# Kernel optimization log

Hardware: AMD Instinct MI355X
Metric: run time of the kernel (lower is better)

## Reference

```python
import jax, jax.numpy as jnp
import numpy as np

B, D_IN, E, H, V = 4096, 4096, 2048, 2048, 32000


def setup_inputs() -> dict:
    key = jax.random.key(0)
    ks = jax.random.split(key, 24)
    s = 0.02
    p = lambda k, shape: (jax.random.normal(k, shape, dtype=jnp.float32) * s)
    return {
        "input": jax.random.normal(ks[0], (B, D_IN), dtype=jnp.float32),
        "hidden": jnp.zeros((B, H), dtype=jnp.float32),
        "cell": jnp.zeros((B, H), dtype=jnp.float32),
        # embedding linear (input_size -> emb_size), stored as [in, out]
        "We": p(ks[1], (D_IN, E)), "be": p(ks[2], (E,)),
        # x-to-gate linears (emb -> hidden)
        "Wf": p(ks[3], (E, H)), "bf": p(ks[4], (H,)),
        "Wi": p(ks[5], (E, H)), "bi": p(ks[6], (H,)),
        "Wc": p(ks[7], (E, H)), "bc": p(ks[8], (H,)),
        "Wo": p(ks[9], (E, H)), "bo": p(ks[10], (H,)),
        # hidden-to-gate linears (hidden -> hidden)
        "Uf": p(ks[11], (H, H)), "bhf": p(ks[12], (H,)),
        "Ui": p(ks[13], (H, H)), "bhi": p(ks[14], (H,)),
        "Uc": p(ks[15], (H, H)), "bhc": p(ks[16], (H,)),
        "Uo": p(ks[17], (H, H)), "bho": p(ks[18], (H,)),
        # output head (hidden -> output_size)
        "Wend": p(ks[19], (H, V)), "bend": p(ks[20], (V,)),
    }


def reference(input, hidden, cell,
              We, be, Wf, bf, Wi, bi, Wc, bc, Wo, bo,
              Uf, bhf, Ui, bhi, Uc, bhc, Uo, bho, Wend, bend):
    # embedded = Linear(input)
    emb = input @ We + be                                  # [B, E]
    f = jax.nn.sigmoid(emb @ Wf + bf + hidden @ Uf + bhf)  # forget gate [B, H]
    i = jax.nn.sigmoid(emb @ Wi + bi + hidden @ Ui + bhi)  # input gate
    g = jnp.tanh(emb @ Wc + bc + hidden @ Uc + bhc)        # candidate cell
    new_cell = f * cell + i * g
    o = jax.nn.sigmoid(emb @ Wo + bo + hidden @ Uo + bho)  # output gate
    new_hidden = o * jnp.tanh(new_cell)
    out = jax.nn.log_softmax(new_hidden @ Wend + bend, axis=1)  # [B, V]
    return (out, new_hidden, new_cell)
```

## Files before the change

### kernel.cpp

```cpp
#include <hip/hip_runtime.h>
#include <stdint.h>

#define B_DIM 4096
#define DIN   4096
#define E_DIM 2048
#define H_DIM 2048
#define V_DIM 32000

typedef __attribute__((ext_vector_type(8))) short s8v;
typedef __attribute__((ext_vector_type(4))) float f4v;
typedef __attribute__((ext_vector_type(4))) int   i4v;
typedef __attribute__((ext_vector_type(8))) int   i8v;
typedef __attribute__((ext_vector_type(4))) uint  u4v;
typedef __attribute__((ext_vector_type(4))) float f4n;

__device__ __forceinline__ ushort f2bf(float f) {
    union { float f; uint32_t u; } v; v.f = f;
    uint32_t u = v.u;
    return (ushort)((u + 0x7FFFu + ((u >> 16) & 1u)) >> 16);
}
__device__ __forceinline__ float bf2f(ushort h) {
    union { uint32_t u; float f; } v; v.u = ((uint32_t)h) << 16;
    return v.f;
}

__device__ __forceinline__ uint8_t f2fp8(float x) {
    union { float f; uint32_t u; } v; v.f = x;
    uint8_t sign = (uint8_t)((v.u >> 24) & 0x80u);
    uint32_t a = v.u & 0x7FFFFFFFu;
    if (a >= 0x43E00000u) return sign | 0x7E;
    uint32_t r = a + 0x0007FFFFu + ((a >> 20) & 1u);
    int e = (int)(r >> 23) - 127 + 7;
    if (e <= 0) {
        float s = fabsf(x);
        int q = (int)(s * 512.0f + 0.5f);
        if (q > 7) q = 7;
        return sign | (uint8_t)q;
    }
    uint32_t m = (r >> 20) & 7u;
    uint8_t b = (uint8_t)((e << 3) | m);
    if (b == 0x7F) b = 0x7E;
    return sign | b;
}

__global__ void k_cvt(const float* __restrict__ src, ushort* __restrict__ dst, int n4) {
    int i = blockIdx.x * blockDim.x + threadIdx.x;
    if (i >= n4) return;
    float4 v = *(const float4*)(src + (size_t)i * 4);
    ushort4 o;
    o.x = f2bf(v.x); o.y = f2bf(v.y); o.z = f2bf(v.z); o.w = f2bf(v.w);
    *(ushort4*)(dst + (size_t)i * 4) = o;
}

__global__ void k_cvt_hidden(const float* __restrict__ src, ushort* __restrict__ dst) {
    int i = blockIdx.x * blockDim.x + threadIdx.x;
    int b = i >> 9;
    int c = (i & 511) << 2;
    float4 v = *(const float4*)(src + (size_t)b * H_DIM + c);
    ushort4 o;
    o.x = f2bf(v.x); o.y = f2bf(v.y); o.z = f2bf(v.z); o.w = f2bf(v.w);
    *(ushort4*)(dst + (size_t)b * 4096 + 2048 + c) = o;
}

__global__ void k_transpose_bf16(const float* __restrict__ src, ushort* __restrict__ dst,
                                 int srcCols, int dstStride, int dstRowOff, int dstColOff) {
    __shared__ float tile[32][33];
    int tx = threadIdx.x, ty = threadIdx.y;
    int n0 = blockIdx.x * 32, k0 = blockIdx.y * 32;
#pragma unroll
    for (int i = 0; i < 4; i++)
        tile[ty + 8 * i][tx] = src[(size_t)(k0 + ty + 8 * i) * srcCols + n0 + tx];
    __syncthreads();
#pragma unroll
    for (int i = 0; i < 4; i++) {
        int n = ty + 8 * i;
        dst[(size_t)(dstRowOff + n0 + n) * dstStride + dstColOff + k0 + tx] = f2bf(tile[tx][n]);
    }
}

__global__ void k_transpose_fp8(const float* __restrict__ src, uint8_t* __restrict__ dst,
                                int srcCols, int dstStride) {
    __shared__ float tile[32][33];
    int tx = threadIdx.x, ty = threadIdx.y;
    int n0 = blockIdx.x * 32, k0 = blockIdx.y * 32;
#pragma unroll
    for (int i = 0; i < 4; i++)
        tile[ty + 8 * i][tx] = src[(size_t)(k0 + ty + 8 * i) * srcCols + n0 + tx];
    __syncthreads();
#pragma unroll
    for (int i = 0; i < 4; i++) {
        int n = ty + 8 * i;
        dst[(size_t)(n0 + n) * dstStride + k0 + tx] = f2fp8(tile[tx][n] * 32.0f);
    }
}

__global__ void k_transpose_gate8(const float* __restrict__ W0, const float* __restrict__ W1,
                                  const float* __restrict__ W2, const float* __restrict__ W3,
                                  const float* __restrict__ U0, const float* __restrict__ U1,
                                  const float* __restrict__ U2, const float* __restrict__ U3,
                                  ushort* __restrict__ dst) {
    const float* srcs[8] = {W0, W1, W2, W3, U0, U1, U2, U3};
    int z = blockIdx.z;
    const float* src = srcs[z];
    int g = z & 3;
    int dstColOff = (z >> 2) << 11;
    __shared__ float tile[32][33];
    int tx = threadIdx.x, ty = threadIdx.y;
    int n0 = blockIdx.x * 32, k0 = blockIdx.y * 32;
#pragma unroll
    for (int i = 0; i < 4; i++)
        tile[ty + 8 * i][tx] = src[(size_t)(k0 + ty + 8 * i) * H_DIM + n0 + tx];
    __syncthreads();
#pragma unroll
    for (int i = 0; i < 4; i++) {
        int h = n0 + ty + 8 * i;
        int drow = ((h >> 6) << 8) + ((g >> 1) << 7) + (((h >> 4) & 3) << 5) + ((g & 1) << 4) + (h & 15);
        dst[(size_t)drow * 4096 + dstColOff + k0 + tx] = f2bf(tile[tx][ty + 8 * i]);
    }
}

__global__ void k_biaspack(const float* __restrict__ b0, const float* __restrict__ bh0,
                           const float* __restrict__ b1, const float* __restrict__ bh1,
                           const float* __restrict__ b2, const float* __restrict__ bh2,
                           const float* __restrict__ b3, const float* __restrict__ bh3,
                           float* __restrict__ out) {
    int h = blockIdx.x * blockDim.x + threadIdx.x;
    if (h >= H_DIM) return;
    int base = ((h >> 6) << 8) + (((h >> 4) & 3) << 5) + (h & 15);
    out[base]             = b0[h] + bh0[h];
    out[base + 16]        = b1[h] + bh1[h];
    out[base + 128]       = b2[h] + bh2[h];
    out[base + 128 + 16]  = b3[h] + bh3[h];
}

template<int OUT_BF16>
__global__ __launch_bounds__(256, 2)
void k_gemm_bt(const ushort* __restrict__ A, const ushort* __restrict__ Bt,
               void* __restrict__ Cv, const float* __restrict__ bias,
               int M, int N, int K, int lda, int ldb, int ldc) {
    __shared__ __align__(16) ushort ldsA[128 * 64];
    __shared__ __align__(16) ushort ldsB[128 * 64];
    const int t = threadIdx.x;
    const int wid = t >> 6, lane = t & 63;

    int nwg = gridDim.x;
    int bid = blockIdx.x;
    int wg  = (bid & 7) * (nwg >> 3) + (bid >> 3);
    int NT  = N >> 7;
    int mt  = wg / NT, nt = wg - mt * NT;
    int m0  = mt << 7, n0 = nt << 7;

    f4v acc[4][4];
#pragma unroll
    for (int i = 0; i < 4; i++)
#pragma unroll
        for (int j = 0; j < 4; j++) acc[i][j] = (f4v){0.f, 0.f, 0.f, 0.f};

    const int wr = wid >> 1, wc = wid & 1;

    const int kTiles = K >> 6;
    for (int kt = 0; kt < kTiles; ++kt) {
#pragma unroll
        for (int c = 0; c < 4; ++c) {
            int idx = c * 256 + wid * 64 + lane;
            int row = idx >> 3;
            int kb  = (idx & 7) << 4;
            const ushort* gA = A  + (size_t)(m0 + row) * lda + (kt << 6) + (kb >> 1);
            const ushort* gB = Bt + (size_t)(n0 + row) * ldb + (kt << 6) + (kb >> 1);
            char* lA = (char*)ldsA + (size_t)(c * 256 + wid * 64) * 16;
            char* lB = (char*)ldsB + (size_t)(c * 256 + wid * 64) * 16;
            __builtin_amdgcn_global_load_lds((const __attribute__((address_space(1))) void*)gA,
                                             (__attribute__((address_space(3))) void*)lA, 16, 0, 0);
            __builtin_amdgcn_global_load_lds((const __attribute__((address_space(1))) void*)gB,
                                             (__attribute__((address_space(3))) void*)lB, 16, 0, 0);
        }
        __syncthreads();

#pragma unroll
        for (int ks = 0; ks < 2; ++ks) {
            s8v af[4], bfr[4];
#pragma unroll
            for (int m = 0; m < 4; ++m) {
                int r = wr * 64 + m * 16 + (lane & 15);
                int kb = ks * 64 + ((lane >> 4) << 4);
                af[m] = *(const s8v*)((const char*)ldsA + r * 128 + kb);
            }
#pragma unroll
            for (int n = 0; n < 4; ++n) {
                int r = wc * 64 + n * 16 + (lane & 15);
                int kb = ks * 64 + ((lane >> 4) << 4);
                bfr[n] = *(const s8v*)((const char*)ldsB + r * 128 + kb);
            }
#pragma unroll
            for (int m = 0; m < 4; ++m)
#pragma unroll
                for (int n = 0; n < 4; ++n)
                    acc[m][n] = __builtin_amdgcn_mfma_f32_16x16x32_bf16(af[m], bfr[n], acc[m][n], 0, 0, 0);
        }
        __syncthreads();
    }

#pragma unroll
    for (int n = 0; n < 4; ++n) {
        int cg = n0 + wc * 64 + n * 16 + (lane & 15);
        float bv = bias[cg];
#pragma unroll
        for (int m = 0; m < 4; ++m) {
            int rbase = m0 + wr * 64 + m * 16 + ((lane >> 4) << 2);
#pragma unroll
            for (int r = 0; r < 4; ++r) {
                float v = acc[m][n][r] + bv;
                if (OUT_BF16)
                    ((ushort*)Cv)[(size_t)(rbase + r) * ldc + cg] = f2bf(v);
                else
                    ((float*)Cv)[(size_t)(rbase + r) * ldc + cg] = v;
            }
        }
    }
}

template<int EPI>
__global__ __launch_bounds__(512, 2)
void k_gemm256(const ushort* __restrict__ A, const ushort* __restrict__ Bt,
               void* __restrict__ Cv, const float* __restrict__ bias,
               int N, int K, int lda, int ldb, int ldc,
               const float* __restrict__ cell, float* __restrict__ outH,
               float* __restrict__ outC, uint8_t* __restrict__ hidF8,
               float2* __restrict__ partials, int ncb) {
    __shared__ __align__(16) ushort ldsA[2][256 * 64];
    __shared__ __align__(16) ushort ldsB[2][256 * 64];
    const int t = threadIdx.x;
    const int wid = t >> 6, lane = t & 63;
    const int wr = wid >> 2, wc = wid & 3;

    int nwg = gridDim.x, bid = blockIdx.x;
    int wg = (bid & 7) * (nwg >> 3) + (bid >> 3);
    int NT = N >> 8;
    int mt = wg / NT, nt = wg - mt * NT;
    int m0 = mt << 8, n0 = nt << 8;

    int offA[4], offB[4];
#pragma unroll
    for (int cc = 0; cc < 4; ++cc) {
        int idx = cc * 512 + t;
        int row = idx >> 3;
        int col = ((idx & 7) ^ (row & 7)) << 3;
        offA[cc] = (m0 + row) * lda + col;
        offB[cc] = (n0 + row) * ldb + col;
    }

#define GLOAD(GP, LP) __builtin_amdgcn_global_load_lds(                                   \
        (const __attribute__((address_space(1))) void*)(GP),                              \
        (__attribute__((address_space(3))) void*)(LP), 16, 0, 0)
#define STAGE_HA(BUF, KT, H) do {                                                         \
    GLOAD(A + offA[(H)*2]     + ((KT) << 6), &ldsA[BUF][(((H)*2)*512 + (wid<<6)) * 8]);   \
    GLOAD(A + offA[(H)*2 + 1] + ((KT) << 6), &ldsA[BUF][(((H)*2+1)*512 + (wid<<6)) * 8]); \
} while (0)
#define STAGE_HB(BUF, KT, H) do {                                                         \
    GLOAD(Bt + offB[(H)*2]     + ((KT) << 6), &ldsB[BUF][(((H)*2)*512 + (wid<<6)) * 8]);  \
    GLOAD(Bt + offB[(H)*2 + 1] + ((KT) << 6), &ldsB[BUF][(((H)*2+1)*512 + (wid<<6)) * 8]);\
} while (0)

    f4v acc[8][4];
#pragma unroll
    for (int i = 0; i < 8; i++)
#pragma unroll
        for (int j = 0; j < 4; j++) acc[i][j] = (f4v){0.f, 0.f, 0.f, 0.f};

    s8v af[4][2], bfA[2][2], bfB[2][2];
    const int swz = (lane & 7) << 4;
    const int kcol = (lane >> 4) << 4;

#define READ_A(BUF, MH) do {                                                              \
    _Pragma("unroll")                                                                     \
    for (int m_ = 0; m_ < 4; ++m_) {                                                      \
        int row = (MH)*128 + wr*64 + m_*16 + (lane & 15);                                 \
        _Pragma("unroll")                                                                 \
        for (int ks_ = 0; ks_ < 2; ++ks_)                                                 \
            af[m_][ks_] = *(const s8v*)((const char*)&ldsA[BUF][0] + row * 128 +          \
                                        ((ks_*64 + kcol) ^ swz));                         \
    } } while (0)
#define READ_B(BUF, NH, DST) do {                                                         \
    _Pragma("unroll")                                                                     \
    for (int n_ = 0; n_ < 2; ++n_) {                                                      \
        int row = (NH)*128 + wc*32 + n_*16 + (lane & 15);                                 \
        _Pragma("unroll")                                                                 \
        for (int ks_ = 0; ks_ < 2; ++ks_)                                                 \
            DST[n_][ks_] = *(const s8v*)((const char*)&ldsB[BUF][0] + row * 128 +         \
                                         ((ks_*64 + kcol) ^ swz));                        \
    } } while (0)
#define MFMA_Q(MH, NH, BF) do {                                                           \
    __builtin_amdgcn_s_setprio(1);                                                        \
    _Pragma("unroll")                                                                     \
    for (int m_ = 0; m_ < 4; ++m_)                                                        \
    _Pragma("unroll")                                                                     \
    for (int n_ = 0; n_ < 2; ++n_)                                                        \
    _Pragma("unroll")                                                                     \
    for (int ks_ = 0; ks_ < 2; ++ks_)                                                     \
        acc[(MH)*4 + m_][(NH)*2 + n_] = __builtin_amdgcn_mfma_f32_16x16x32_bf16(          \
            af[m_][ks_], BF[n_][ks_], acc[(MH)*4 + m_][(NH)*2 + n_], 0, 0, 0);            \
    __builtin_amdgcn_s_setprio(0);                                                        \
} while (0)
#define MEMBAR asm volatile("" ::: "memory")
#define BAR() do { MEMBAR; __builtin_amdgcn_s_barrier(); MEMBAR; } while (0)
#define WAITLGKM0() do { asm volatile("s_waitcnt lgkmcnt(0)" ::: "memory");               \
                         __builtin_amdgcn_sched_barrier(0); } while (0)

    const int kTiles = K >> 6;
    STAGE_HA(0, 0, 0); STAGE_HB(0, 0, 0); STAGE_HB(0, 0, 1); STAGE_HA(0, 0, 1);
    STAGE_HA(1, 1, 0); STAGE_HB(1, 1, 0); STAGE_HB(1, 1, 1); STAGE_HA(1, 1, 1);
    asm volatile("s_waitcnt vmcnt(6)" ::: "memory");
    BAR();

    for (int kt = 0; kt < kTiles; ++kt) {
        const int buf = kt & 1;
        const bool pf = (kt + 2 < kTiles);
        READ_A(buf, 0); READ_B(buf, 0, bfA);
        asm volatile("s_waitcnt lgkmcnt(8)" ::: "memory");
        BAR(); WAITLGKM0();
        MFMA_Q(0, 0, bfA);
        BAR();
        READ_B(buf, 1, bfB);
        if (pf) STAGE_HA(buf, kt + 2, 0);
        BAR(); WAITLGKM0();
        MFMA_Q(0, 1, bfB);
        BAR();
        READ_A(buf, 1);
        if (pf) STAGE_HB(buf, kt + 2, 0);
        BAR(); WAITLGKM0();
        MFMA_Q(1, 1, bfB);
        BAR();
        if (pf) { STAGE_HB(buf, kt + 2, 1); STAGE_HA(buf, kt + 2, 1); }
        MFMA_Q(1, 0, bfA);
        if (pf) asm volatile("s_waitcnt vmcnt(8)" ::: "memory");
        else    asm volatile("s_waitcnt vmcnt(0)" ::: "memory");
        BAR();
    }

    if (EPI == 0) {
    } else {
        int h = (n0 >> 2) + wc * 16 + (lane & 15);
        float bv[4];
#pragma unroll
        for (int j = 0; j < 4; ++j)
            bv[j] = bias[n0 + (j >> 1) * 128 + wc * 32 + (j & 1) * 16 + (lane & 15)];
#pragma unroll
        for (int mh = 0; mh < 2; ++mh)
#pragma unroll
        for (int m = 0; m < 4; ++m) {
            int rb = m0 + mh * 128 + wr * 64 + m * 16 + ((lane >> 4) << 2);
#pragma unroll
            for (int r = 0; r < 4; ++r) {
                int b = rb + r;
                float pf_ = acc[mh * 4 + m][0][r] + bv[0];
                float pi_ = acc[mh * 4 + m][1][r] + bv[1];
                float pc_ = acc[mh * 4 + m][2][r] + bv[2];
                float po_ = acc[mh * 4 + m][3][r] + bv[3];
                float fg = 1.f / (1.f + __expf(-pf_));
                float ig = 1.f / (1.f + __expf(-pi_));
                float gg = tanhf(pc_);
                float og = 1.f / (1.f + __expf(-po_));
                size_t off = (size_t)b * H_DIM + h;
                float nc = fg * cell[off] + ig * gg;
                float nh = og * tanhf(nc);
                outC[off] = nc;
                outH[off] = nh;
                hidF8[off] = f2fp8(nh * 8.0f);
            }
        }
    }
#undef GLOAD
#undef STAGE_HA
#undef STAGE_HB
#undef READ_A
#undef READ_B
#undef MFMA_Q
#undef MEMBAR
#undef BAR
#undef WAITLGKM0
}

__global__ __launch_bounds__(256, 3)
void k_gemm_mx(const uint8_t* __restrict__ A, const uint8_t* __restrict__ Bt,
               ushort* __restrict__ Lbf, const float* __restrict__ bias,
               float2* __restrict__ partials, int N, int K, int ldc, int ncb) {
    __shared__ __align__(16) uint8_t ldsA[128 * 128];
    __shared__ __align__(16) uint8_t ldsB[128 * 128];
    const int t = threadIdx.x;
    const int wid = t >> 6, lane = t & 63;
    const int wrr = wid >> 1, wcc = wid & 1;

    int bid = blockIdx.x;
    int mt  = ((bid & 7) << 2) | ((bid >> 3) & 3);
    int nt  = bid >> 5;
    int m0  = mt << 7, n0 = nt << 7;

    int offA[4], offB[4];
#pragma unroll
    for (int c = 0; c < 4; ++c) {
        int idx = c * 256 + t;
        int row = idx >> 3;
        int cb  = ((idx & 7) ^ (row & 7)) << 4;
        offA[c] = (m0 + row) * K + cb;
        offB[c] = (n0 + row) * K + cb;
    }

    f4v acc[4][4];
#pragma unroll
    for (int i = 0; i < 4; ++i)
#pragma unroll
        for (int j = 0; j < 4; ++j) acc[i][j] = (f4v){0.f, 0.f, 0.f, 0.f};

    const int l15 = lane & 15;
    const int sw  = (lane & 7) << 4;
    const int o0  = ((lane >> 4) << 5) ^ sw;
    const int o1  = o0 ^ 16;

    const int kTiles = K >> 7;
    for (int kt = 0; kt < kTiles; ++kt) {
#pragma unroll
        for (int c = 0; c < 4; ++c) {
            __builtin_amdgcn_global_load_lds(
                (const __attribute__((address_space(1))) void*)(A + offA[c] + (kt << 7)),
                (__attribute__((address_space(3))) void*)&ldsA[(c * 256 + wid * 64) * 16], 16, 0, 0);
            __builtin_amdgcn_global_load_lds(
                (const __attribute__((address_space(1))) void*)(Bt + offB[c] + (kt << 7)),
                (__attribute__((address_space(3))) void*)&ldsB[(c * 256 + wid * 64) * 16], 16, 0, 0);
        }
        __syncthreads();

        i8v af[4], bf[4];
#pragma unroll
        for (int m = 0; m < 4; ++m) {
            int row = wrr * 64 + m * 16 + l15;
            i4v lo = *(const i4v*)&ldsA[row * 128 + o0];
            i4v hi = *(const i4v*)&ldsA[row * 128 + o1];
            af[m] = __builtin_shufflevector(lo, hi, 0, 1, 2, 3, 4, 5, 6, 7);
        }
#pragma unroll
        for (int n = 0; n < 4; ++n) {
            int row = wcc * 64 + n * 16 + l15;
            i4v lo = *(const i4v*)&ldsB[row * 128 + o0];
            i4v hi = *(const i4v*)&ldsB[row * 128 + o1];
            bf[n] = __builtin_shufflevector(lo, hi, 0, 1, 2, 3, 4, 5, 6, 7);
        }
#pragma unroll
        for (int m = 0; m < 4; ++m)
#pragma unroll
            for (int n = 0; n < 4; ++n)
                acc[m][n] = __builtin_amdgcn_mfma_scale_f32_16x16x128_f8f6f4(
                    af[m], bf[n], acc[m][n], 0, 0, 0, 124, 0, 122);
        __syncthreads();
    }

    float bv[4];
#pragma unroll
    for (int n = 0; n < 4; ++n) bv[n] = bias[n0 + wcc * 64 + n * 16 + l15];
    float2* sm = (float2*)ldsA;
#pragma unroll
    for (int m = 0; m < 4; ++m) {
#pragma unroll
        for (int r = 0; r < 4; ++r) {
            int rl = wrr * 64 + m * 16 + ((lane >> 4) << 2) + r;
            float v[4];
#pragma unroll
            for (int n = 0; n < 4; ++n) v[n] = acc[m][n][r] + bv[n];
            size_t cr = (size_t)(m0 + rl) * ldc + n0 + wcc * 64 + l15;
            __builtin_nontemporal_store(f2bf(v[0]), &Lbf[cr]);
            __builtin_nontemporal_store(f2bf(v[1]), &Lbf[cr + 16]);
            __builtin_nontemporal_store(f2bf(v[2]), &Lbf[cr + 32]);
            __builtin_nontemporal_store(f2bf(v[3]), &Lbf[cr + 48]);
            float mx = fmaxf(fmaxf(v[0], v[1]), fmaxf(v[2], v[3]));
            float ss = __expf(v[0] - mx) + __expf(v[1] - mx) +
                       __expf(v[2] - mx) + __expf(v[3] - mx);
#pragma unroll
            for (int off = 1; off < 16; off <<= 1) {
                float mo = __shfl_xor(mx, off);
                float so = __shfl_xor(ss, off);
                float nm = fmaxf(mx, mo);
                ss = ss * __expf(mx - nm) + so * __expf(mo - nm);
                mx = nm;
            }
            if (l15 == 0) sm[wcc * 128 + rl] = make_float2(mx, ss);
        }
    }
    __syncthreads();
    if (t < 128) {
        float2 a = sm[t], b = sm[128 + t];
        float M = fmaxf(a.x, b.x);
        float S = a.y * __expf(a.x - M) + b.y * __expf(b.x - M);
        partials[(size_t)(m0 + t) * ncb + nt] = make_float2(M, S);
    }
}

__global__ void k_lsefin(const float2* __restrict__ part, float* __restrict__ lse, int ncb) {
    int row = blockIdx.x;
    int l = threadIdx.x;
    float M = -1e30f, S = 0.f;
    for (int i = l; i < ncb; i += 64) {
        float2 p = part[(size_t)row * ncb + i];
        float nm = fmaxf(M, p.x);
        S = S * __expf(M - nm) + p.y * __expf(p.x - nm);
        M = nm;
    }
#pragma unroll
    for (int off = 1; off < 64; off <<= 1) {
        float Mo = __shfl_xor(M, off);
        float So = __shfl_xor(S, off);
        float nm = fmaxf(M, Mo);
        S = S * __expf(M - nm) + So * __expf(Mo - nm);
        M = nm;
    }
    if (l == 0) lse[row] = M + logf(S);
}

__global__ void k_norm(const ushort* __restrict__ Lbf, const float* __restrict__ lse,
                       float* __restrict__ out) {
    int b = blockIdx.y;
    int c8 = blockIdx.x * blockDim.x + threadIdx.x;
    if (c8 >= V_DIM / 8) return;
    float l = lse[b];
    const u4v* src = (const u4v*)(Lbf + (size_t)b * V_DIM + (size_t)c8 * 8);
    u4v pv = __builtin_nontemporal_load(src);
    f4n q0, q1;
    q0.x = bf2f((ushort)(pv.x & 0xFFFF)) - l;
    q0.y = bf2f((ushort)(pv.x >> 16)) - l;
    q0.z = bf2f((ushort)(pv.y & 0xFFFF)) - l;
    q0.w = bf2f((ushort)(pv.y >> 16)) - l;
    q1.x = bf2f((ushort)(pv.z & 0xFFFF)) - l;
    q1.y = bf2f((ushort)(pv.z >> 16)) - l;
    q1.z = bf2f((ushort)(pv.w & 0xFFFF)) - l;
    q1.w = bf2f((ushort)(pv.w >> 16)) - l;
    float* dst = out + (size_t)b * V_DIM + (size_t)c8 * 8;
    __builtin_nontemporal_store(q0, (f4n*)dst);
    __builtin_nontemporal_store(q1, (f4n*)(dst + 4));
}

extern "C" void kernel_launch(void* const* d_in, const int* in_sizes, int n_in,
                              void* d_out, int out_size, void* d_ws, size_t ws_size,
                              hipStream_t stream) {
    const float* in_input  = (const float*)d_in[0];
    const float* in_hidden = (const float*)d_in[1];
    const float* in_cell   = (const float*)d_in[2];
    const float* We   = (const float*)d_in[3];
    const float* be   = (const float*)d_in[4];
    const float* Wf   = (const float*)d_in[5];
    const float* bfv  = (const float*)d_in[6];
    const float* Wi   = (const float*)d_in[7];
    const float* biv  = (const float*)d_in[8];
    const float* Wc   = (const float*)d_in[9];
    const float* bcv  = (const float*)d_in[10];
    const float* Wo   = (const float*)d_in[11];
    const float* bov  = (const float*)d_in[12];
    const float* Uf   = (const float*)d_in[13];
    const float* bhf  = (const float*)d_in[14];
    const float* Ui   = (const float*)d_in[15];
    const float* bhi  = (const float*)d_in[16];
    const float* Uc   = (const float*)d_in[17];
    const float* bhc  = (const float*)d_in[18];
    const float* Uo   = (const float*)d_in[19];
    const float* bho  = (const float*)d_in[20];
    const float* Wend = (const float*)d_in[21];
    const float* bend = (const float*)d_in[22];

    char* ws = (char*)d_ws;
    const size_t oWendF8 = 0;
    const size_t oHidF8  = oWendF8 + (size_t)V_DIM * H_DIM;
    const size_t oBias2  = oHidF8 + (size_t)B_DIM * H_DIM;
    const size_t oLse    = oBias2 + 4 * H_DIM * 4;
    const size_t oPart   = oLse + B_DIM * 4;
    const size_t oR      = oPart + (size_t)B_DIM * 250 * 8;
    const size_t oAin    = oR;
    const size_t oWeT    = oAin + (size_t)B_DIM * DIN * 2;
    const size_t oA2     = oWeT + (size_t)E_DIM * DIN * 2;
    const size_t oWUT    = oA2  + (size_t)B_DIM * 4096 * 2;

    uint8_t* WendF8 = (uint8_t*)(ws + oWendF8);
    uint8_t* hidF8  = (uint8_t*)(ws + oHidF8);
    float*   bias2  = (float*)(ws + oBias2);
    float*   lse    = (float*)(ws + oLse);
    float2*  part   = (float2*)(ws + oPart);
    ushort*  Lbf    = (ushort*)(ws + oR);
    ushort*  Ain    = (ushort*)(ws + oAin);
    ushort*  WeT    = (ushort*)(ws + oWeT);
    ushort*  A2     = (ushort*)(ws + oA2);
    ushort*  WUT    = (ushort*)(ws + oWUT);

    float* out  = (float*)d_out;
    float* outH = out + (size_t)B_DIM * V_DIM;
    float* outC = outH + (size_t)B_DIM * H_DIM;

    const int NCB = V_DIM / 128;

    dim3 blk256(256), blk512(512), blk64(64);

    k_cvt<<<dim3((B_DIM * DIN / 4) / 256), blk256, 0, stream>>>(in_input, Ain, B_DIM * DIN / 4);
    k_cvt_hidden<<<dim3((B_DIM * H_DIM / 4) / 256), blk256, 0, stream>>>(in_hidden, A2);

    dim3 tb(32, 8);
    k_transpose_bf16<<<dim3(E_DIM / 32, DIN / 32), tb, 0, stream>>>(We, WeT, E_DIM, DIN, 0, 0);
    k_transpose_gate8<<<dim3(H_DIM / 32, E_DIM / 32, 8), tb, 0, stream>>>(
        Wf, Wi, Wc, Wo, Uf, Ui, Uc, Uo, WUT);
    k_transpose_fp8<<<dim3(V_DIM / 32, H_DIM / 32), tb, 0, stream>>>(Wend, WendF8, V_DIM, H_DIM);
    k_biaspack<<<dim3(H_DIM / 256), blk256, 0, stream>>>(bfv, bhf, biv, bhi, bcv, bhc, bov, bho, bias2);

    k_gemm_bt<1><<<dim3((B_DIM / 128) * (E_DIM / 128)), blk256, 0, stream>>>(
        Ain, WeT, A2, be, B_DIM, E_DIM, DIN, DIN, DIN, 4096);

    k_gemm256<2><<<dim3((B_DIM / 256) * (8192 / 256)), blk512, 0, stream>>>(
        A2, WUT, nullptr, bias2, 8192, 4096, 4096, 4096, 0,
        in_cell, outH, outC, hidF8, nullptr, 0);

    k_gemm_mx<<<dim3((B_DIM / 128) * (V_DIM / 128)), blk256, 0, stream>>>(
        hidF8, WendF8, Lbf, bend, part, V_DIM, H_DIM, V_DIM, NCB);

    k_lsefin<<<dim3(B_DIM), blk64, 0, stream>>>(part, lse, NCB);
    k_norm<<<dim3(16, B_DIM), blk256, 0, stream>>>(Lbf, lse, out);
}
```

Measured before the change: 1.221 ms.

## Double-buffer LDS in MX fp8 output GEMM with two-tile prefetch

The output-head fp8 GEMM kernel now keeps two LDS buffers and issues the global-to-LDS loads for tile kt+2 while the MFMAs for tile kt run, using explicit vmcnt waits and raw barriers in place of full __syncthreads. MFMA issue priority is also raised during compute. This is meant to hide global load latency behind matrix math. In exchange LDS use doubles to 64KB, so the occupancy hint drops from 3 to 2 blocks per CU.

```diff
diff --git a/kernel.cpp b/kernel.cpp
--- a/kernel.cpp
+++ b/kernel.cpp
@@ -380,12 +380,12 @@
 #undef WAITLGKM0
 }
 
-__global__ __launch_bounds__(256, 3)
+__global__ __launch_bounds__(256, 2)
 void k_gemm_mx(const uint8_t* __restrict__ A, const uint8_t* __restrict__ Bt,
                ushort* __restrict__ Lbf, const float* __restrict__ bias,
                float2* __restrict__ partials, int N, int K, int ldc, int ncb) {
-    __shared__ __align__(16) uint8_t ldsA[128 * 128];
-    __shared__ __align__(16) uint8_t ldsB[128 * 128];
+    __shared__ __align__(16) uint8_t ldsA[2][128 * 128];
+    __shared__ __align__(16) uint8_t ldsB[2][128 * 128];
     const int t = threadIdx.x;
     const int wid = t >> 6, lane = t & 63;
     const int wrr = wid >> 1, wcc = wid & 1;
@@ -405,6 +405,19 @@
         offB[c] = (n0 + row) * K + cb;
     }
 
+#define STAGE_MX(BUF, KT) do {                                                            \
+    _Pragma("unroll")                                                                     \
+    for (int c_ = 0; c_ < 4; ++c_) {                                                      \
+        __builtin_amdgcn_global_load_lds(                                                 \
+            (const __attribute__((address_space(1))) void*)(A + offA[c_] + ((KT) << 7)),  \
+            (__attribute__((address_space(3))) void*)&ldsA[BUF][(c_ * 256 + wid * 64) * 16], \
+            16, 0, 0);                                                                    \
+        __builtin_amdgcn_global_load_lds(                                                 \
+            (const __attribute__((address_space(1))) void*)(Bt + offB[c_] + ((KT) << 7)), \
+            (__attribute__((address_space(3))) void*)&ldsB[BUF][(c_ * 256 + wid * 64) * 16], \
+            16, 0, 0);                                                                    \
+    } } while (0)
+
     f4v acc[4][4];
 #pragma unroll
     for (int i = 0; i < 4; ++i)
@@ -417,46 +430,50 @@
     const int o1  = o0 ^ 16;
 
     const int kTiles = K >> 7;
+    STAGE_MX(0, 0);
+    STAGE_MX(1, 1);
+    asm volatile("s_waitcnt vmcnt(8)" ::: "memory");
+    __builtin_amdgcn_s_barrier();
+
     for (int kt = 0; kt < kTiles; ++kt) {
-#pragma unroll
-        for (int c = 0; c < 4; ++c) {
-            __builtin_amdgcn_global_load_lds(
-                (const __attribute__((address_space(1))) void*)(A + offA[c] + (kt << 7)),
-                (__attribute__((address_space(3))) void*)&ldsA[(c * 256 + wid * 64) * 16], 16, 0, 0);
-            __builtin_amdgcn_global_load_lds(
-                (const __attribute__((address_space(1))) void*)(Bt + offB[c] + (kt << 7)),
-                (__attribute__((address_space(3))) void*)&ldsB[(c * 256 + wid * 64) * 16], 16, 0, 0);
-        }
-        __syncthreads();
-
+        const int buf = kt & 1;
+        const bool pf = (kt + 2 < kTiles);
         i8v af[4], bf[4];
 #pragma unroll
         for (int m = 0; m < 4; ++m) {
             int row = wrr * 64 + m * 16 + l15;
-            i4v lo = *(const i4v*)&ldsA[row * 128 + o0];
-            i4v hi = *(const i4v*)&ldsA[row * 128 + o1];
+            i4v lo = *(const i4v*)&ldsA[buf][row * 128 + o0];
+            i4v hi = *(const i4v*)&ldsA[buf][row * 128 + o1];
             af[m] = __builtin_shufflevector(lo, hi, 0, 1, 2, 3, 4, 5, 6, 7);
         }
 #pragma unroll
         for (int n = 0; n < 4; ++n) {
             int row = wcc * 64 + n * 16 + l15;
-            i4v lo = *(const i4v*)&ldsB[row * 128 + o0];
-            i4v hi = *(const i4v*)&ldsB[row * 128 + o1];
+            i4v lo = *(const i4v*)&ldsB[buf][row * 128 + o0];
+            i4v hi = *(const i4v*)&ldsB[buf][row * 128 + o1];
             bf[n] = __builtin_shufflevector(lo, hi, 0, 1, 2, 3, 4, 5, 6, 7);
         }
+        asm volatile("s_waitcnt lgkmcnt(0)" ::: "memory");
+        __builtin_amdgcn_sched_barrier(0);
+        __builtin_amdgcn_s_barrier();
+        if (pf) STAGE_MX(buf, kt + 2);
+        __builtin_amdgcn_s_setprio(1);
 #pragma unroll
         for (int m = 0; m < 4; ++m)
 #pragma unroll
             for (int n = 0; n < 4; ++n)
                 acc[m][n] = __builtin_amdgcn_mfma_scale_f32_16x16x128_f8f6f4(
                     af[m], bf[n], acc[m][n], 0, 0, 0, 124, 0, 122);
-        __syncthreads();
+        __builtin_amdgcn_s_setprio(0);
+        if (pf)                   asm volatile("s_waitcnt vmcnt(8)" ::: "memory");
+        else if (kt + 1 < kTiles) asm volatile("s_waitcnt vmcnt(0)" ::: "memory");
+        __builtin_amdgcn_s_barrier();
     }
 
     float bv[4];
 #pragma unroll
     for (int n = 0; n < 4; ++n) bv[n] = bias[n0 + wcc * 64 + n * 16 + l15];
-    float2* sm = (float2*)ldsA;
+    float2* sm = (float2*)&ldsA[0][0];
 #pragma unroll
     for (int m = 0; m < 4; ++m) {
 #pragma unroll
@@ -491,6 +508,7 @@
         float S = a.y * __expf(a.x - M) + b.y * __expf(b.x - M);
         partials[(size_t)(m0 + t) * ncb + nt] = make_float2(M, S);
     }
+#undef STAGE_MX
 }
 
 __global__ void k_lsefin(const float2* __restrict__ part, float* __restrict__ lse, int ncb) {
```

New measurement: 1.257 ms. +2.9%, slower.
